# Kernel tuning notes

Measured on AMD Instinct MI355X. Metric: run time of the kernel, lower is better.

The kernel has to match this reference:

```python
import jax, jax.numpy as jnp
import numpy as np
import math

HIDDEN = 1024
HEADS = 16
HEAD_DIM = HIDDEN // HEADS
BASE = 10000.0


def _rope_tables(seq_len):
    inv_freq = 1.0 / (BASE ** (jnp.arange(0, HEAD_DIM, 2, dtype=jnp.float32) / HEAD_DIM))
    t = jnp.arange(seq_len, dtype=jnp.float32)
    freqs = t[:, None] * inv_freq[None, :]  # [S, D/2]
    return jnp.cos(freqs), jnp.sin(freqs)


def _apply_rope(x, cos, sin):
    # x: [B, H, S, D]; interleaved even/odd pairs
    x1, x2 = x[..., 0::2], x[..., 1::2]
    r1 = x1 * cos - x2 * sin
    r2 = x1 * sin + x2 * cos
    out = jnp.stack([r1, r2], axis=-1)  # [B,H,S,D/2,2]
    return out.reshape(x.shape)


def setup_inputs() -> dict:
    key = jax.random.key(0)
    ks = jax.random.split(key, 11)
    B, S = 2, 2048
    scale = 1.0 / math.sqrt(HIDDEN)
    mk = lambda k: (jax.random.normal(k, (HIDDEN, HIDDEN), jnp.float32) * scale)
    return {
        "query": jax.random.normal(ks[0], (B, S, HIDDEN), jnp.float32),
        "key": jax.random.normal(ks[1], (B, S, HIDDEN), jnp.float32),
        "value": jax.random.normal(ks[2], (B, S, HIDDEN), jnp.float32),
        "Wq": mk(ks[3]), "bq": jnp.zeros((HIDDEN,), jnp.float32),
        "Wk": mk(ks[4]), "bk": jnp.zeros((HIDDEN,), jnp.float32),
        "Wv": mk(ks[5]), "bv": jnp.zeros((HIDDEN,), jnp.float32),
        "Wo": mk(ks[6]), "bo": jnp.zeros((HIDDEN,), jnp.float32),
    }


def reference(query, key, value, Wq, bq, Wk, bk, Wv, bv, Wo, bo):
    B, S, _ = query.shape
    # projections (torch Linear: x @ W.T + b)
    def proj(x, W, b):
        y = jnp.einsum('bsh,oh->bso', x, W) + b
        return y.reshape(B, S, HEADS, HEAD_DIM).transpose(0, 2, 1, 3)  # [B,H,S,D]
    Q = proj(query, Wq, bq)
    K = proj(key, Wk, bk)
    V = proj(value, Wv, bv)

    cos, sin = _rope_tables(S)  # [S, D/2]
    Q = _apply_rope(Q, cos, sin)
    K = _apply_rope(K, cos, sin)

    scores = jnp.einsum('bhqd,bhkd->bhqk', Q, K) / math.sqrt(HEAD_DIM)
    causal = jnp.tril(jnp.ones((S, S), dtype=bool))
    scores = jnp.where(causal, scores, jnp.float32(-1e9))
    attention_weights = jax.nn.softmax(scores, axis=-1)  # [B,H,S,S]

    attn_out = jnp.einsum('bhqk,bhkd->bhqd', attention_weights, V)
    attn_out = attn_out.transpose(0, 2, 1, 3).reshape(B, S, HIDDEN)
    output = jnp.einsum('bsh,oh->bso', attn_out, Wo) + bo
    return output, attention_weights
```

## Files before the change

kernel.cpp:

```cpp
#include <hip/hip_runtime.h>
#include <hip/hip_bf16.h>
#include <math.h>

typedef __attribute__((ext_vector_type(4))) float  f32x4;
typedef __attribute__((ext_vector_type(8))) __bf16 bf16x8;
typedef __attribute__((ext_vector_type(4))) __bf16 bf16x4;

#define HIDDEN 1024
#define HEADS 16
#define HDIM 64
#define BATCH 2
#define SEQ 2048
#define ROWS (BATCH*SEQ)
#define BH (BATCH*HEADS)
#define OUT0_ELEMS ((size_t)ROWS*HIDDEN)
#define PW_ELEMS   ((size_t)BH*SEQ*SEQ)

__device__ __forceinline__ void gload_lds16(const void* g, void* l) {
    __builtin_amdgcn_global_load_lds(
        (const __attribute__((address_space(1))) void*)g,
        (__attribute__((address_space(3))) void*)l,
        16, 0, 0);
}

__global__ void cast_f32_bf16(const float* __restrict__ in, __bf16* __restrict__ out, int n4) {
    int i = blockIdx.x * blockDim.x + threadIdx.x;
    if (i >= n4) return;
    float4 v = ((const float4*)in)[i];
    bf16x4 o = { (__bf16)v.x, (__bf16)v.y, (__bf16)v.z, (__bf16)v.w };
    ((bf16x4*)out)[i] = o;
}

__global__ void rope_tables(float* __restrict__ cosT, float* __restrict__ sinT) {
    int i = blockIdx.x * blockDim.x + threadIdx.x;
    if (i >= SEQ * 32) return;
    int s = i >> 5, f = i & 31;
    float inv = (float)pow(10000.0, -(double)f / 32.0);
    float ang = (float)s * inv;
    cosT[i] = cosf(ang);
    sinT[i] = sinf(ang);
}

__global__ __launch_bounds__(256) void gemm_bt(const __bf16* __restrict__ A,
                                               const __bf16* __restrict__ Bt,
                                               const float* __restrict__ bias,
                                               float* __restrict__ C,
                                               int M, int N, int K) {
    __shared__ __bf16 As[128 * 32];
    __shared__ __bf16 Bs[128 * 32];
    const int tid = threadIdx.x, lane = tid & 63, wid = tid >> 6;
    const int wr = wid >> 1, wc = wid & 1;
    const int fr = lane & 15, fq = lane >> 4;
    const int row0 = blockIdx.x * 128, col0 = blockIdx.y * 128;

    f32x4 acc[4][4] = {};
    for (int k0 = 0; k0 < K; k0 += 32) {
        #pragma unroll
        for (int c2 = 0; c2 < 2; ++c2) {
            int ob = wid * 2048 + c2 * 1024;
            int o  = ob + lane * 16;
            int r  = o >> 6, cb = o & 63;
            gload_lds16(A  + (size_t)(row0 + r) * K + k0 + (cb >> 1), (char*)As + ob);
            gload_lds16(Bt + (size_t)(col0 + r) * K + k0 + (cb >> 1), (char*)Bs + ob);
        }
        __syncthreads();
        bf16x8 af[4], bfr[4];
        #pragma unroll
        for (int m = 0; m < 4; ++m) af[m]  = *(const bf16x8*)(As + (wr * 64 + m * 16 + fr) * 32 + fq * 8);
        #pragma unroll
        for (int n = 0; n < 4; ++n) bfr[n] = *(const bf16x8*)(Bs + (wc * 64 + n * 16 + fr) * 32 + fq * 8);
        #pragma unroll
        for (int m = 0; m < 4; ++m)
            #pragma unroll
            for (int n = 0; n < 4; ++n)
                acc[m][n] = __builtin_amdgcn_mfma_f32_16x16x32_bf16(af[m], bfr[n], acc[m][n], 0, 0, 0);
        __syncthreads();
    }
    #pragma unroll
    for (int m = 0; m < 4; ++m)
        #pragma unroll
        for (int n = 0; n < 4; ++n) {
            int col = col0 + wc * 64 + n * 16 + fr;
            float bv = bias[col];
            #pragma unroll
            for (int j = 0; j < 4; ++j) {
                int row = row0 + wr * 64 + m * 16 + fq * 4 + j;
                C[(size_t)row * N + col] = acc[m][n][j] + bv;
            }
        }
}

__global__ void rope_relayout(const float* __restrict__ proj,
                              const float* __restrict__ cosT, const float* __restrict__ sinT,
                              __bf16* __restrict__ out) {
    int idx = blockIdx.x * blockDim.x + threadIdx.x;
    if (idx >= ROWS * 512) return;
    int m = idx >> 9, p = idx & 511;
    int h = p >> 5, i = p & 31;
    int b = m >> 11, s = m & 2047;
    float x1 = proj[(size_t)m * HIDDEN + h * 64 + 2 * i];
    float x2 = proj[(size_t)m * HIDDEN + h * 64 + 2 * i + 1];
    float c = cosT[s * 32 + i], sn = sinT[s * 32 + i];
    size_t o = ((size_t)(b * HEADS + h) * SEQ + s) * 64 + 2 * i;
    out[o]     = (__bf16)(x1 * c - x2 * sn);
    out[o + 1] = (__bf16)(x1 * sn + x2 * c);
}

__global__ void v_relayout(const float* __restrict__ proj, __bf16* __restrict__ Vt) {
    int idx = blockIdx.x * blockDim.x + threadIdx.x;
    if (idx >= ROWS * HIDDEN) return;
    int m = idx >> 10, c = idx & 1023;
    int h = c >> 6, d = c & 63;
    int b = m >> 11, s = m & 2047;
    Vt[((size_t)(b * HEADS + h) * 64 + d) * SEQ + s] = (__bf16)proj[idx];
}

__global__ __launch_bounds__(256) void attn_scores(const __bf16* __restrict__ Qb,
                                                   const __bf16* __restrict__ Kb,
                                                   float* __restrict__ P,
                                                   float* __restrict__ m_arr,
                                                   float* __restrict__ l_arr) {
    const int qt = blockIdx.x, bh = blockIdx.y;
    const int lane = threadIdx.x & 63, w = threadIdx.x >> 6;
    const int fr = lane & 15, fq = lane >> 4;
    const int rowBase = qt * 64 + w * 16;

    const size_t qoff = ((size_t)bh * SEQ + rowBase + fr) * 64;
    bf16x8 aq0 = *(const bf16x8*)(Qb + qoff + fq * 8);
    bf16x8 aq1 = *(const bf16x8*)(Qb + qoff + 32 + fq * 8);

    float mrow[4] = { -INFINITY, -INFINITY, -INFINITY, -INFINITY };
    float lrow[4] = { 0.f, 0.f, 0.f, 0.f };
    const int nkt16 = (rowBase / 32 + 1) * 2;

    for (int kt = 0; kt < nkt16; ++kt) {
        const size_t koff = ((size_t)bh * SEQ + kt * 16 + fr) * 64;
        bf16x8 bk0 = *(const bf16x8*)(Kb + koff + fq * 8);
        bf16x8 bk1 = *(const bf16x8*)(Kb + koff + 32 + fq * 8);
        f32x4 sc = { 0.f, 0.f, 0.f, 0.f };
        sc = __builtin_amdgcn_mfma_f32_16x16x32_bf16(aq0, bk0, sc, 0, 0, 0);
        sc = __builtin_amdgcn_mfma_f32_16x16x32_bf16(aq1, bk1, sc, 0, 0, 0);
        int col = kt * 16 + fr;
        #pragma unroll
        for (int j = 0; j < 4; ++j) {
            int row = rowBase + fq * 4 + j;
            float s = sc[j] * 0.125f;
            if (col > row) s = -1e9f;
            float nm = fmaxf(mrow[j], s);
            lrow[j] = lrow[j] * __expf(mrow[j] - nm) + __expf(s - nm);
            mrow[j] = nm;
            P[((size_t)bh * SEQ + row) * SEQ + col] = s;
        }
    }
    #pragma unroll
    for (int j = 0; j < 4; ++j) {
        float m = mrow[j], l = lrow[j];
        #pragma unroll
        for (int d = 1; d < 16; d <<= 1) {
            float mo = __shfl_xor(m, d, 64);
            float lo = __shfl_xor(l, d, 64);
            float nm = fmaxf(m, mo);
            l = l * __expf(m - nm) + lo * __expf(mo - nm);
            m = nm;
        }
        if (fr == 0) {
            int row = rowBase + fq * 4 + j;
            m_arr[(size_t)bh * SEQ + row] = m;
            l_arr[(size_t)bh * SEQ + row] = l;
        }
    }
}

__global__ __launch_bounds__(256) void attn_pv(float* __restrict__ P,
                                               const __bf16* __restrict__ Vt,
                                               const float* __restrict__ m_arr,
                                               const float* __restrict__ l_arr,
                                               __bf16* __restrict__ aout) {
    const int qt = blockIdx.x, bh = blockIdx.y;
    const int lane = threadIdx.x & 63, w = threadIdx.x >> 6;
    const int fr = lane & 15, fq = lane >> 4;
    const int rowBase = qt * 64 + w * 16;
    const int row = rowBase + fr;
    const float m = m_arr[(size_t)bh * SEQ + row];
    const float linv = 1.0f / l_arr[(size_t)bh * SEQ + row];
    float* Pr = P + ((size_t)bh * SEQ + row) * SEQ;
    const int nkt32 = rowBase / 32 + 1;

    f32x4 acc[4] = {};
    for (int kt = 0; kt < nkt32; ++kt) {
        float4 s0 = *(const float4*)(Pr + kt * 32 + fq * 8);
        float4 s1 = *(const float4*)(Pr + kt * 32 + fq * 8 + 4);
        float p0 = __expf(s0.x - m) * linv;
        float p1 = __expf(s0.y - m) * linv;
        float p2 = __expf(s0.z - m) * linv;
        float p3 = __expf(s0.w - m) * linv;
        float p4 = __expf(s1.x - m) * linv;
        float p5 = __expf(s1.y - m) * linv;
        float p6 = __expf(s1.z - m) * linv;
        float p7 = __expf(s1.w - m) * linv;
        *(float4*)(Pr + kt * 32 + fq * 8)     = float4{ p0, p1, p2, p3 };
        *(float4*)(Pr + kt * 32 + fq * 8 + 4) = float4{ p4, p5, p6, p7 };
        bf16x8 pa = { (__bf16)p0, (__bf16)p1, (__bf16)p2, (__bf16)p3,
                      (__bf16)p4, (__bf16)p5, (__bf16)p6, (__bf16)p7 };
        #pragma unroll
        for (int nd = 0; nd < 4; ++nd) {
            bf16x8 bv = *(const bf16x8*)(Vt + ((size_t)bh * 64 + nd * 16 + fr) * SEQ + kt * 32 + fq * 8);
            acc[nd] = __builtin_amdgcn_mfma_f32_16x16x32_bf16(pa, bv, acc[nd], 0, 0, 0);
        }
    }
    const int b = bh >> 4, h = bh & 15;
    #pragma unroll
    for (int nd = 0; nd < 4; ++nd)
        #pragma unroll
        for (int j = 0; j < 4; ++j) {
            int qrow = rowBase + fq * 4 + j;
            int d = nd * 16 + fr;
            aout[((size_t)(b * SEQ + qrow)) * HIDDEN + h * 64 + d] = (__bf16)acc[nd][j];
        }
}

extern "C" void kernel_launch(void* const* d_in, const int* in_sizes, int n_in,
                              void* d_out, int out_size, void* d_ws, size_t ws_size,
                              hipStream_t stream) {
    const float* query = (const float*)d_in[0];
    const float* key   = (const float*)d_in[1];
    const float* value = (const float*)d_in[2];
    const float* Wq = (const float*)d_in[3];
    const float* bq = (const float*)d_in[4];
    const float* Wk = (const float*)d_in[5];
    const float* bk = (const float*)d_in[6];
    const float* Wv = (const float*)d_in[7];
    const float* bv = (const float*)d_in[8];
    const float* Wo = (const float*)d_in[9];
    const float* bo = (const float*)d_in[10];

    float* out0 = (float*)d_out;
    float* P    = (float*)d_out + OUT0_ELEMS;

    char* p = (char*)d_ws;
    auto alloc = [&](size_t bytes) { char* r = p; p += (bytes + 255) & ~(size_t)255; return r; };
    float*  cosT = (float*)alloc(SEQ * 32 * 4);
    float*  sinT = (float*)alloc(SEQ * 32 * 4);
    __bf16* Xq   = (__bf16*)alloc(OUT0_ELEMS * 2);
    __bf16* Xk   = (__bf16*)alloc(OUT0_ELEMS * 2);
    __bf16* Xv   = (__bf16*)alloc(OUT0_ELEMS * 2);
    __bf16* Wqb  = (__bf16*)alloc((size_t)HIDDEN * HIDDEN * 2);
    __bf16* Wkb  = (__bf16*)alloc((size_t)HIDDEN * HIDDEN * 2);
    __bf16* Wvb  = (__bf16*)alloc((size_t)HIDDEN * HIDDEN * 2);
    __bf16* Wob  = (__bf16*)alloc((size_t)HIDDEN * HIDDEN * 2);
    float*  proj = (float*)alloc(OUT0_ELEMS * 4);
    __bf16* Qb   = (__bf16*)alloc((size_t)BH * SEQ * 64 * 2);
    __bf16* Kb   = (__bf16*)alloc((size_t)BH * SEQ * 64 * 2);
    __bf16* Vt   = (__bf16*)alloc((size_t)BH * SEQ * 64 * 2);
    float*  m_arr = (float*)alloc((size_t)BH * SEQ * 4);
    float*  l_arr = (float*)alloc((size_t)BH * SEQ * 4);
    __bf16* aout = (__bf16*)alloc(OUT0_ELEMS * 2);

    hipMemsetAsync(P, 0, PW_ELEMS * 4, stream);

    rope_tables<<<(SEQ * 32 + 255) / 256, 256, 0, stream>>>(cosT, sinT);

    cast_f32_bf16<<<(ROWS * HIDDEN / 4 + 255) / 256, 256, 0, stream>>>(query, Xq, ROWS * HIDDEN / 4);
    cast_f32_bf16<<<(ROWS * HIDDEN / 4 + 255) / 256, 256, 0, stream>>>(key,   Xk, ROWS * HIDDEN / 4);
    cast_f32_bf16<<<(ROWS * HIDDEN / 4 + 255) / 256, 256, 0, stream>>>(value, Xv, ROWS * HIDDEN / 4);
    cast_f32_bf16<<<(HIDDEN * HIDDEN / 4 + 255) / 256, 256, 0, stream>>>(Wq, Wqb, HIDDEN * HIDDEN / 4);
    cast_f32_bf16<<<(HIDDEN * HIDDEN / 4 + 255) / 256, 256, 0, stream>>>(Wk, Wkb, HIDDEN * HIDDEN / 4);
    cast_f32_bf16<<<(HIDDEN * HIDDEN / 4 + 255) / 256, 256, 0, stream>>>(Wv, Wvb, HIDDEN * HIDDEN / 4);
    cast_f32_bf16<<<(HIDDEN * HIDDEN / 4 + 255) / 256, 256, 0, stream>>>(Wo, Wob, HIDDEN * HIDDEN / 4);

    dim3 ggemm(ROWS / 128, HIDDEN / 128);

    gemm_bt<<<ggemm, 256, 0, stream>>>(Xq, Wqb, bq, proj, ROWS, HIDDEN, HIDDEN);
    rope_relayout<<<(ROWS * 512 + 255) / 256, 256, 0, stream>>>(proj, cosT, sinT, Qb);
    gemm_bt<<<ggemm, 256, 0, stream>>>(Xk, Wkb, bk, proj, ROWS, HIDDEN, HIDDEN);
    rope_relayout<<<(ROWS * 512 + 255) / 256, 256, 0, stream>>>(proj, cosT, sinT, Kb);
    gemm_bt<<<ggemm, 256, 0, stream>>>(Xv, Wvb, bv, proj, ROWS, HIDDEN, HIDDEN);
    v_relayout<<<(ROWS * HIDDEN + 255) / 256, 256, 0, stream>>>(proj, Vt);

    dim3 gattn(SEQ / 64, BH);
    attn_scores<<<gattn, 256, 0, stream>>>(Qb, Kb, P, m_arr, l_arr);
    attn_pv<<<gattn, 256, 0, stream>>>(P, Vt, m_arr, l_arr, aout);

    gemm_bt<<<ggemm, 256, 0, stream>>>(aout, Wob, bo, out0, ROWS, HIDDEN, HIDDEN);
}
```

Before: 1.226 ms.

## Fuse QKV GEMMs, fuse attention passes, drop memset, LDS transpose for V

Merges the three projection GEMMs into one launch over a concatenated output, and combines the Q/K RoPE relayouts into one kernel. V is transposed through shared memory instead of with scattered stores. The score and PV kernels are merged into one kernel that recomputes QK^T in a second pass, so the fp32 score matrix is no longer written and read back. The full-size memset of the attention weights is replaced by zero-filling only the masked tail of each row. This mainly targets the large HBM traffic on the 512MB probability output, at the cost of doing the score MFMAs twice.

```diff
diff --git a/kernel.cpp b/kernel.cpp
--- a/kernel.cpp
+++ b/kernel.cpp
@@ -8,13 +8,12 @@
 
 #define HIDDEN 1024
 #define HEADS 16
-#define HDIM 64
 #define BATCH 2
 #define SEQ 2048
 #define ROWS (BATCH*SEQ)
 #define BH (BATCH*HEADS)
+#define NQ 3072
 #define OUT0_ELEMS ((size_t)ROWS*HIDDEN)
-#define PW_ELEMS   ((size_t)BH*SEQ*SEQ)
 
 __device__ __forceinline__ void gload_lds16(const void* g, void* l) {
     __builtin_amdgcn_global_load_lds(
@@ -39,6 +38,64 @@
     float ang = (float)s * inv;
     cosT[i] = cosf(ang);
     sinT[i] = sinf(ang);
+}
+
+__global__ __launch_bounds__(256) void gemm_qkv(const __bf16* __restrict__ Xq,
+                                                const __bf16* __restrict__ Xk,
+                                                const __bf16* __restrict__ Xv,
+                                                const __bf16* __restrict__ Wq,
+                                                const __bf16* __restrict__ Wk,
+                                                const __bf16* __restrict__ Wv,
+                                                const float* __restrict__ bq,
+                                                const float* __restrict__ bk,
+                                                const float* __restrict__ bv,
+                                                float* __restrict__ C) {
+    __shared__ __bf16 As[128 * 32];
+    __shared__ __bf16 Bs[128 * 32];
+    const int tid = threadIdx.x, lane = tid & 63, wid = tid >> 6;
+    const int wr = wid >> 1, wc = wid & 1;
+    const int fr = lane & 15, fq = lane >> 4;
+    const int row0 = blockIdx.x * 128, col0 = blockIdx.y * 128;
+    const int sel = col0 >> 10, colr = col0 & 1023;
+    const __bf16* A    = sel == 0 ? Xq : sel == 1 ? Xk : Xv;
+    const __bf16* Bt   = sel == 0 ? Wq : sel == 1 ? Wk : Wv;
+    const float*  bias = sel == 0 ? bq : sel == 1 ? bk : bv;
+
+    f32x4 acc[4][4] = {};
+    for (int k0 = 0; k0 < HIDDEN; k0 += 32) {
+        #pragma unroll
+        for (int c2 = 0; c2 < 2; ++c2) {
+            int ob = wid * 2048 + c2 * 1024;
+            int o  = ob + lane * 16;
+            int r  = o >> 6, cb = o & 63;
+            gload_lds16(A  + (size_t)(row0 + r) * HIDDEN + k0 + (cb >> 1), (char*)As + ob);
+            gload_lds16(Bt + (size_t)(colr + r) * HIDDEN + k0 + (cb >> 1), (char*)Bs + ob);
+        }
+        __syncthreads();
+        bf16x8 af[4], bfr[4];
+        #pragma unroll
+        for (int m = 0; m < 4; ++m) af[m]  = *(const bf16x8*)(As + (wr * 64 + m * 16 + fr) * 32 + fq * 8);
+        #pragma unroll
+        for (int n = 0; n < 4; ++n) bfr[n] = *(const bf16x8*)(Bs + (wc * 64 + n * 16 + fr) * 32 + fq * 8);
+        #pragma unroll
+        for (int m = 0; m < 4; ++m)
+            #pragma unroll
+            for (int n = 0; n < 4; ++n)
+                acc[m][n] = __builtin_amdgcn_mfma_f32_16x16x32_bf16(af[m], bfr[n], acc[m][n], 0, 0, 0);
+        __syncthreads();
+    }
+    #pragma unroll
+    for (int m = 0; m < 4; ++m)
+        #pragma unroll
+        for (int n = 0; n < 4; ++n) {
+            int off = wc * 64 + n * 16 + fr;
+            float bvv = bias[colr + off];
+            #pragma unroll
+            for (int j = 0; j < 4; ++j) {
+                int row = row0 + wr * 64 + m * 16 + fq * 4 + j;
+                C[(size_t)row * NQ + col0 + off] = acc[m][n][j] + bvv;
+            }
+        }
 }
 
 __global__ __launch_bounds__(256) void gemm_bt(const __bf16* __restrict__ A,
@@ -90,71 +147,99 @@
         }
 }
 
-__global__ void rope_relayout(const float* __restrict__ proj,
-                              const float* __restrict__ cosT, const float* __restrict__ sinT,
-                              __bf16* __restrict__ out) {
+__global__ void rope_qk(const float* __restrict__ proj,
+                        const float* __restrict__ cosT, const float* __restrict__ sinT,
+                        __bf16* __restrict__ Qb, __bf16* __restrict__ Kb) {
     int idx = blockIdx.x * blockDim.x + threadIdx.x;
     if (idx >= ROWS * 512) return;
     int m = idx >> 9, p = idx & 511;
     int h = p >> 5, i = p & 31;
     int b = m >> 11, s = m & 2047;
-    float x1 = proj[(size_t)m * HIDDEN + h * 64 + 2 * i];
-    float x2 = proj[(size_t)m * HIDDEN + h * 64 + 2 * i + 1];
     float c = cosT[s * 32 + i], sn = sinT[s * 32 + i];
+    size_t pbase = (size_t)m * NQ + h * 64 + 2 * i;
+    float q1 = proj[pbase],        q2 = proj[pbase + 1];
+    float k1 = proj[pbase + 1024], k2 = proj[pbase + 1025];
     size_t o = ((size_t)(b * HEADS + h) * SEQ + s) * 64 + 2 * i;
-    out[o]     = (__bf16)(x1 * c - x2 * sn);
-    out[o + 1] = (__bf16)(x1 * sn + x2 * c);
-}
-
-__global__ void v_relayout(const float* __restrict__ proj, __bf16* __restrict__ Vt) {
-    int idx = blockIdx.x * blockDim.x + threadIdx.x;
-    if (idx >= ROWS * HIDDEN) return;
-    int m = idx >> 10, c = idx & 1023;
-    int h = c >> 6, d = c & 63;
-    int b = m >> 11, s = m & 2047;
-    Vt[((size_t)(b * HEADS + h) * 64 + d) * SEQ + s] = (__bf16)proj[idx];
-}
-
-__global__ __launch_bounds__(256) void attn_scores(const __bf16* __restrict__ Qb,
-                                                   const __bf16* __restrict__ Kb,
-                                                   float* __restrict__ P,
-                                                   float* __restrict__ m_arr,
-                                                   float* __restrict__ l_arr) {
+    Qb[o]     = (__bf16)(q1 * c - q2 * sn);
+    Qb[o + 1] = (__bf16)(q1 * sn + q2 * c);
+    Kb[o]     = (__bf16)(k1 * c - k2 * sn);
+    Kb[o + 1] = (__bf16)(k1 * sn + k2 * c);
+}
+
+__global__ __launch_bounds__(256) void v_transpose(const float* __restrict__ proj,
+                                                   __bf16* __restrict__ Vt) {
+    __shared__ float T[64][65];
+    const int s0 = blockIdx.x * 64, bh = blockIdx.y;
+    const int b = bh >> 4, h = bh & 15;
+    const int t = threadIdx.x;
+    {
+        int r = t >> 2, f4 = t & 3;
+        const float* src = proj + (size_t)(b * SEQ + s0 + r) * NQ + 2048 + h * 64;
+        #pragma unroll
+        for (int i = 0; i < 4; ++i)
+            *(float4*)&T[r][f4 * 4 + i * 16] = *(const float4*)(src + f4 * 4 + i * 16);
+    }
+    __syncthreads();
+    {
+        int d = t >> 2, slot = t & 3;
+        __bf16* dst = Vt + ((size_t)bh * 64 + d) * SEQ + s0 + slot * 16;
+        #pragma unroll
+        for (int half = 0; half < 2; ++half) {
+            bf16x8 o;
+            #pragma unroll
+            for (int i = 0; i < 8; ++i) o[i] = (__bf16)T[slot * 16 + half * 8 + i][d];
+            *(bf16x8*)(dst + half * 8) = o;
+        }
+    }
+}
+
+__global__ __launch_bounds__(256) void attn_fused(const __bf16* __restrict__ Qb,
+                                                  const __bf16* __restrict__ Kb,
+                                                  const __bf16* __restrict__ Vt,
+                                                  float* __restrict__ P,
+                                                  __bf16* __restrict__ aout) {
+    __shared__ __bf16 Pl[4][2][16 * 40];
     const int qt = blockIdx.x, bh = blockIdx.y;
     const int lane = threadIdx.x & 63, w = threadIdx.x >> 6;
     const int fr = lane & 15, fq = lane >> 4;
     const int rowBase = qt * 64 + w * 16;
 
     const size_t qoff = ((size_t)bh * SEQ + rowBase + fr) * 64;
-    bf16x8 aq0 = *(const bf16x8*)(Qb + qoff + fq * 8);
-    bf16x8 aq1 = *(const bf16x8*)(Qb + qoff + 32 + fq * 8);
-
-    float mrow[4] = { -INFINITY, -INFINITY, -INFINITY, -INFINITY };
-    float lrow[4] = { 0.f, 0.f, 0.f, 0.f };
-    const int nkt16 = (rowBase / 32 + 1) * 2;
-
-    for (int kt = 0; kt < nkt16; ++kt) {
-        const size_t koff = ((size_t)bh * SEQ + kt * 16 + fr) * 64;
-        bf16x8 bk0 = *(const bf16x8*)(Kb + koff + fq * 8);
-        bf16x8 bk1 = *(const bf16x8*)(Kb + koff + 32 + fq * 8);
-        f32x4 sc = { 0.f, 0.f, 0.f, 0.f };
-        sc = __builtin_amdgcn_mfma_f32_16x16x32_bf16(aq0, bk0, sc, 0, 0, 0);
-        sc = __builtin_amdgcn_mfma_f32_16x16x32_bf16(aq1, bk1, sc, 0, 0, 0);
-        int col = kt * 16 + fr;
-        #pragma unroll
-        for (int j = 0; j < 4; ++j) {
-            int row = rowBase + fq * 4 + j;
-            float s = sc[j] * 0.125f;
-            if (col > row) s = -1e9f;
-            float nm = fmaxf(mrow[j], s);
-            lrow[j] = lrow[j] * __expf(mrow[j] - nm) + __expf(s - nm);
-            mrow[j] = nm;
-            P[((size_t)bh * SEQ + row) * SEQ + col] = s;
+    const bf16x8 aq0 = *(const bf16x8*)(Qb + qoff + fq * 8);
+    const bf16x8 aq1 = *(const bf16x8*)(Qb + qoff + 32 + fq * 8);
+
+    const __bf16* Kbh = Kb + (size_t)bh * SEQ * 64;
+    const __bf16* Vbh = Vt + (size_t)bh * 64 * SEQ;
+    float* Pbh = P + (size_t)bh * SEQ * SEQ;
+
+    const int nkt = rowBase / 32 + 1;
+
+    float mr[4] = { -INFINITY, -INFINITY, -INFINITY, -INFINITY };
+    float lr[4] = { 0.f, 0.f, 0.f, 0.f };
+    for (int kt = 0; kt < nkt; ++kt) {
+        #pragma unroll
+        for (int t2 = 0; t2 < 2; ++t2) {
+            const __bf16* kp = Kbh + (size_t)(kt * 32 + t2 * 16 + fr) * 64;
+            bf16x8 bk0 = *(const bf16x8*)(kp + fq * 8);
+            bf16x8 bk1 = *(const bf16x8*)(kp + 32 + fq * 8);
+            f32x4 sc = { 0.f, 0.f, 0.f, 0.f };
+            sc = __builtin_amdgcn_mfma_f32_16x16x32_bf16(aq0, bk0, sc, 0, 0, 0);
+            sc = __builtin_amdgcn_mfma_f32_16x16x32_bf16(aq1, bk1, sc, 0, 0, 0);
+            const int col = kt * 32 + t2 * 16 + fr;
+            #pragma unroll
+            for (int j = 0; j < 4; ++j) {
+                int row = rowBase + fq * 4 + j;
+                float s = sc[j] * 0.125f;
+                if (col > row) s = -1e9f;
+                float nm = fmaxf(mr[j], s);
+                lr[j] = lr[j] * __expf(mr[j] - nm) + __expf(s - nm);
+                mr[j] = nm;
+            }
         }
     }
     #pragma unroll
     for (int j = 0; j < 4; ++j) {
-        float m = mrow[j], l = lrow[j];
+        float m = mr[j], l = lr[j];
         #pragma unroll
         for (int d = 1; d < 16; d <<= 1) {
             float mo = __shfl_xor(m, d, 64);
@@ -163,59 +248,54 @@
             l = l * __expf(m - nm) + lo * __expf(mo - nm);
             m = nm;
         }
-        if (fr == 0) {
-            int row = rowBase + fq * 4 + j;
-            m_arr[(size_t)bh * SEQ + row] = m;
-            l_arr[(size_t)bh * SEQ + row] = l;
-        }
-    }
-}
-
-__global__ __launch_bounds__(256) void attn_pv(float* __restrict__ P,
-                                               const __bf16* __restrict__ Vt,
-                                               const float* __restrict__ m_arr,
-                                               const float* __restrict__ l_arr,
-                                               __bf16* __restrict__ aout) {
-    const int qt = blockIdx.x, bh = blockIdx.y;
-    const int lane = threadIdx.x & 63, w = threadIdx.x >> 6;
-    const int fr = lane & 15, fq = lane >> 4;
-    const int rowBase = qt * 64 + w * 16;
-    const int row = rowBase + fr;
-    const float m = m_arr[(size_t)bh * SEQ + row];
-    const float linv = 1.0f / l_arr[(size_t)bh * SEQ + row];
-    float* Pr = P + ((size_t)bh * SEQ + row) * SEQ;
-    const int nkt32 = rowBase / 32 + 1;
+        mr[j] = m;
+        lr[j] = 1.0f / l;
+    }
 
     f32x4 acc[4] = {};
-    for (int kt = 0; kt < nkt32; ++kt) {
-        float4 s0 = *(const float4*)(Pr + kt * 32 + fq * 8);
-        float4 s1 = *(const float4*)(Pr + kt * 32 + fq * 8 + 4);
-        float p0 = __expf(s0.x - m) * linv;
-        float p1 = __expf(s0.y - m) * linv;
-        float p2 = __expf(s0.z - m) * linv;
-        float p3 = __expf(s0.w - m) * linv;
-        float p4 = __expf(s1.x - m) * linv;
-        float p5 = __expf(s1.y - m) * linv;
-        float p6 = __expf(s1.z - m) * linv;
-        float p7 = __expf(s1.w - m) * linv;
-        *(float4*)(Pr + kt * 32 + fq * 8)     = float4{ p0, p1, p2, p3 };
-        *(float4*)(Pr + kt * 32 + fq * 8 + 4) = float4{ p4, p5, p6, p7 };
-        bf16x8 pa = { (__bf16)p0, (__bf16)p1, (__bf16)p2, (__bf16)p3,
-                      (__bf16)p4, (__bf16)p5, (__bf16)p6, (__bf16)p7 };
+    for (int kt = 0; kt < nkt; ++kt) {
+        __bf16* pl = &Pl[w][kt & 1][0];
+        #pragma unroll
+        for (int t2 = 0; t2 < 2; ++t2) {
+            const __bf16* kp = Kbh + (size_t)(kt * 32 + t2 * 16 + fr) * 64;
+            bf16x8 bk0 = *(const bf16x8*)(kp + fq * 8);
+            bf16x8 bk1 = *(const bf16x8*)(kp + 32 + fq * 8);
+            f32x4 sc = { 0.f, 0.f, 0.f, 0.f };
+            sc = __builtin_amdgcn_mfma_f32_16x16x32_bf16(aq0, bk0, sc, 0, 0, 0);
+            sc = __builtin_amdgcn_mfma_f32_16x16x32_bf16(aq1, bk1, sc, 0, 0, 0);
+            const int col = kt * 32 + t2 * 16 + fr;
+            #pragma unroll
+            for (int j = 0; j < 4; ++j) {
+                int row = rowBase + fq * 4 + j;
+                float s = sc[j] * 0.125f;
+                if (col > row) s = -1e9f;
+                float p = __expf(s - mr[j]) * lr[j];
+                Pbh[(size_t)row * SEQ + col] = p;
+                pl[(fq * 4 + j) * 40 + t2 * 16 + fr] = (__bf16)p;
+            }
+        }
+        bf16x8 pa = *(const bf16x8*)(pl + fr * 40 + fq * 8);
         #pragma unroll
         for (int nd = 0; nd < 4; ++nd) {
-            bf16x8 bv = *(const bf16x8*)(Vt + ((size_t)bh * 64 + nd * 16 + fr) * SEQ + kt * 32 + fq * 8);
+            bf16x8 bv = *(const bf16x8*)(Vbh + (size_t)(nd * 16 + fr) * SEQ + kt * 32 + fq * 8);
             acc[nd] = __builtin_amdgcn_mfma_f32_16x16x32_bf16(pa, bv, acc[nd], 0, 0, 0);
         }
     }
+
+    {
+        int r = rowBase + (lane >> 2);
+        float4 z = { 0.f, 0.f, 0.f, 0.f };
+        for (int c = nkt * 32 + (lane & 3) * 4; c < SEQ; c += 16)
+            *(float4*)(Pbh + (size_t)r * SEQ + c) = z;
+    }
+
     const int b = bh >> 4, h = bh & 15;
     #pragma unroll
     for (int nd = 0; nd < 4; ++nd)
         #pragma unroll
         for (int j = 0; j < 4; ++j) {
             int qrow = rowBase + fq * 4 + j;
-            int d = nd * 16 + fr;
-            aout[((size_t)(b * SEQ + qrow)) * HIDDEN + h * 64 + d] = (__bf16)acc[nd][j];
+            aout[((size_t)(b * SEQ + qrow)) * HIDDEN + h * 64 + nd * 16 + fr] = (__bf16)acc[nd][j];
         }
 }
 
@@ -248,15 +328,11 @@
     __bf16* Wkb  = (__bf16*)alloc((size_t)HIDDEN * HIDDEN * 2);
     __bf16* Wvb  = (__bf16*)alloc((size_t)HIDDEN * HIDDEN * 2);
     __bf16* Wob  = (__bf16*)alloc((size_t)HIDDEN * HIDDEN * 2);
-    float*  proj = (float*)alloc(OUT0_ELEMS * 4);
+    float*  proj = (float*)alloc((size_t)ROWS * NQ * 4);
     __bf16* Qb   = (__bf16*)alloc((size_t)BH * SEQ * 64 * 2);
     __bf16* Kb   = (__bf16*)alloc((size_t)BH * SEQ * 64 * 2);
     __bf16* Vt   = (__bf16*)alloc((size_t)BH * SEQ * 64 * 2);
-    float*  m_arr = (float*)alloc((size_t)BH * SEQ * 4);
-    float*  l_arr = (float*)alloc((size_t)BH * SEQ * 4);
     __bf16* aout = (__bf16*)alloc(OUT0_ELEMS * 2);
-
-    hipMemsetAsync(P, 0, PW_ELEMS * 4, stream);
 
     rope_tables<<<(SEQ * 32 + 255) / 256, 256, 0, stream>>>(cosT, sinT);
 
@@ -268,18 +344,16 @@
     cast_f32_bf16<<<(HIDDEN * HIDDEN / 4 + 255) / 256, 256, 0, stream>>>(Wv, Wvb, HIDDEN * HIDDEN / 4);
     cast_f32_bf16<<<(HIDDEN * HIDDEN / 4 + 255) / 256, 256, 0, stream>>>(Wo, Wob, HIDDEN * HIDDEN / 4);
 
+    dim3 gqkv(ROWS / 128, NQ / 128);
+    gemm_qkv<<<gqkv, 256, 0, stream>>>(Xq, Xk, Xv, Wqb, Wkb, Wvb, bq, bk, bv, proj);
+
+    rope_qk<<<(ROWS * 512 + 255) / 256, 256, 0, stream>>>(proj, cosT, sinT, Qb, Kb);
+    dim3 gvt(SEQ / 64, BH);
+    v_transpose<<<gvt, 256, 0, stream>>>(proj, Vt);
+
+    dim3 gattn(SEQ / 64, BH);
+    attn_fused<<<gattn, 256, 0, stream>>>(Qb, Kb, Vt, P, aout);
+
     dim3 ggemm(ROWS / 128, HIDDEN / 128);
-
-    gemm_bt<<<ggemm, 256, 0, stream>>>(Xq, Wqb, bq, proj, ROWS, HIDDEN, HIDDEN);
-    rope_relayout<<<(ROWS * 512 + 255) / 256, 256, 0, stream>>>(proj, cosT, sinT, Qb);
-    gemm_bt<<<ggemm, 256, 0, stream>>>(Xk, Wkb, bk, proj, ROWS, HIDDEN, HIDDEN);
-    rope_relayout<<<(ROWS * 512 + 255) / 256, 256, 0, stream>>>(proj, cosT, sinT, Kb);
-    gemm_bt<<<ggemm, 256, 0, stream>>>(Xv, Wvb, bv, proj, ROWS, HIDDEN, HIDDEN);
-    v_relayout<<<(ROWS * HIDDEN + 255) / 256, 256, 0, stream>>>(proj, Vt);
-
-    dim3 gattn(SEQ / 64, BH);
-    attn_scores<<<gattn, 256, 0, stream>>>(Qb, Kb, P, m_arr, l_arr);
-    attn_pv<<<gattn, 256, 0, stream>>>(P, Vt, m_arr, l_arr, aout);
-
     gemm_bt<<<ggemm, 256, 0, stream>>>(aout, Wob, bo, out0, ROWS, HIDDEN, HIDDEN);
 }
```

After: 988.7 us. -19.3%, faster.
